# Kernel tuning notes

Measured on AMD Instinct MI355X. Metric: run time of the kernel, lower is better.

## Reference

```python
import jax, jax.numpy as jnp
import numpy as np

N = 50000       # nodes
E = 150000      # directed edges
NODE_IN = 64
EDGE_IN = 16
D = 32          # node_out_feats
EDGE_HID = 128
STEPS = 3       # num_step_message_passing


def setup_inputs() -> dict:
    key = jax.random.key(0)
    ks = jax.random.split(key, 10)
    s = 0.05
    return {
        "x": jax.random.normal(ks[0], (N, NODE_IN), jnp.float32),
        "edge_index": jax.random.randint(ks[1], (2, E), 0, N),
        "edge_attr": jax.random.normal(ks[2], (E, EDGE_IN), jnp.float32),
        # node_init Linear
        "Wn": jax.random.normal(ks[3], (NODE_IN, D), jnp.float32) * s,
        "bn": jnp.zeros((D,), jnp.float32),
        # edge_network: Linear(edge_in, hid) -> ReLU -> Linear(hid, D*D)
        "We1": jax.random.normal(ks[4], (EDGE_IN, EDGE_HID), jnp.float32) * s,
        "be1": jnp.zeros((EDGE_HID,), jnp.float32),
        "We2": jax.random.normal(ks[5], (EDGE_HID, D * D), jnp.float32) * s,
        "be2": jnp.zeros((D * D,), jnp.float32),
        # NNConv root weight + bias
        "Wroot": jax.random.normal(ks[6], (D, D), jnp.float32) * s,
        "bconv": jnp.zeros((D,), jnp.float32),
        # GRU (gate order r, z, n as in torch)
        "Wih": jax.random.normal(ks[7], (3 * D, D), jnp.float32) * s,
        "Whh": jax.random.normal(ks[8], (3 * D, D), jnp.float32) * s,
        "bih": jnp.zeros((3 * D,), jnp.float32),
        "bhh": jnp.zeros((3 * D,), jnp.float32),
    }


def _gru_cell(xt, h, Wih, Whh, bih, bhh):
    gi = xt @ Wih.T + bih   # [N, 3D]
    gh = h @ Whh.T + bhh    # [N, 3D]
    r = jax.nn.sigmoid(gi[:, :D] + gh[:, :D])
    z = jax.nn.sigmoid(gi[:, D:2 * D] + gh[:, D:2 * D])
    n = jnp.tanh(gi[:, 2 * D:] + r * gh[:, 2 * D:])
    return (1.0 - z) * n + z * h


def reference(x, edge_index, edge_attr, Wn, bn, We1, be1, We2, be2,
              Wroot, bconv, Wih, Whh, bih, bhh):
    src, dst = edge_index[0], edge_index[1]
    # per-edge weight matrices from edge_network (edge_attr fixed across steps)
    Wm = (jax.nn.relu(edge_attr @ We1 + be1) @ We2 + be2).reshape(E, D, D)
    h = jax.nn.relu(x @ Wn + bn)   # node_init
    hid = h                        # GRU hidden state
    for _ in range(STEPS):
        # NNConv: gather -> per-edge matmul -> scatter-add, plus root + bias
        m = jnp.einsum('ei,eio->eo', h[src], Wm)                # [E, D]
        agg = jax.ops.segment_sum(m, dst, num_segments=N)       # [N, D]
        conv = jax.nn.relu(agg + h @ Wroot + bconv)
        hid = _gru_cell(conv, hid, Wih, Whh, bih, bhh)
        h = hid
    return h
```

## Files before the change

### kernel.cpp

```cpp
#include <hip/hip_runtime.h>
#include <hip/hip_bf16.h>

#define N_NODES 50000
#define N_EDGES 150000
#define NODE_IN 64
#define EDGE_IN 16
#define DD 32
#define EHID 128
#define STEPS 3
#define EPB 64

__device__ __forceinline__ ushort f2b(float f) {
    __hip_bfloat16 b = __float2bfloat16(f);
    return *reinterpret_cast<ushort*>(&b);
}

typedef __bf16 bf16x8 __attribute__((ext_vector_type(8)));
typedef float  f32x4  __attribute__((ext_vector_type(4)));

#define LDA  136
#define HPAD 36

__global__ __launch_bounds__(256) void setup(const float* __restrict__ we2,
                                             const float* __restrict__ we1,
                                             const float* __restrict__ wroot,
                                             const float* __restrict__ wih,
                                             const float* __restrict__ whh,
                                             ushort* __restrict__ we2B,
                                             ushort* __restrict__ we1B,
                                             ushort* __restrict__ wgB,
                                             const float* __restrict__ x,
                                             const float* __restrict__ Wn,
                                             const float* __restrict__ bn,
                                             float* __restrict__ h) {
    __shared__ float Wns[NODE_IN * DD];
    __shared__ float bns[DD];
    int b = blockIdx.x, t = threadIdx.x;

    if (b < 70) {
        int i = b * 256 + t;
        if (i < 16384) {
            int l = i & 63, f = i >> 6;
            int kt = f & 3, nt = (f >> 2) & 3, bq = f >> 4;
            int lr = l & 15, lg = l >> 4;
            int n = bq * 64 + nt * 16 + lr;
            int k0 = kt * 32 + lg * 8;
            ushort tmp[8];
#pragma unroll
            for (int j = 0; j < 8; ++j) tmp[j] = f2b(we2[(size_t)(k0 + j) * 1024 + n]);
            *(uint4*)(we2B + (size_t)i * 8) = *(uint4*)tmp;
        } else if (i < 16896) {
            int u = i - 16384;
            int l = u & 63, nt = u >> 6;
            int lr = l & 15, lg = l >> 4;
            int n = nt * 16 + lr;
            ushort tmp[8];
#pragma unroll
            for (int j = 0; j < 8; ++j) {
                int k = lg * 8 + j;
                tmp[j] = (k < EDGE_IN) ? f2b(we1[(size_t)k * EHID + n]) : (ushort)0;
            }
            *(uint4*)(we1B + (size_t)u * 8) = *(uint4*)tmp;
        } else if (i < 17792) {
            int u = i - 16896;
            int l = u & 63;
            int lr = l & 15, lg = l >> 4;
            ushort tmp[8];
            if (u < 128) {
                int nt = u >> 6;
#pragma unroll
                for (int j = 0; j < 8; ++j)
                    tmp[j] = f2b(wroot[(size_t)(lg * 8 + j) * DD + nt * 16 + lr]);
            } else if (u < 512) {
                int nt = (u - 128) >> 6;
#pragma unroll
                for (int j = 0; j < 8; ++j)
                    tmp[j] = f2b(wih[(size_t)(nt * 16 + lr) * DD + lg * 8 + j]);
            } else {
                int nt = (u - 512) >> 6;
#pragma unroll
                for (int j = 0; j < 8; ++j)
                    tmp[j] = f2b(whh[(size_t)(nt * 16 + lr) * DD + lg * 8 + j]);
            }
            *(uint4*)(wgB + (size_t)u * 8) = *(uint4*)tmp;
        }
    } else {
        for (int i = t; i < NODE_IN * DD; i += 256) Wns[i] = Wn[i];
        if (t < DD) bns[t] = bn[t];
        __syncthreads();
        int n = (b - 70) * 256 + t;
        if (n >= N_NODES) return;
        float xr[NODE_IN];
        const float4* xp = (const float4*)(x + (size_t)n * NODE_IN);
#pragma unroll
        for (int q = 0; q < NODE_IN / 4; ++q) *(float4*)&xr[q * 4] = xp[q];
        float out[DD];
#pragma unroll
        for (int o = 0; o < DD; ++o) {
            float s = bns[o];
#pragma unroll
            for (int i = 0; i < NODE_IN; ++i) s += xr[i] * Wns[i * DD + o];
            out[o] = fmaxf(s, 0.f);
        }
        float4* hp = (float4*)(h + (size_t)n * DD);
#pragma unroll
        for (int q = 0; q < DD / 4; ++q) hp[q] = *(float4*)&out[q * 4];
    }
}

__global__ __launch_bounds__(256, 5) void fused_msg(const float* __restrict__ ea,
                                                    const ushort* __restrict__ we1B,
                                                    const float* __restrict__ be1,
                                                    const ushort* __restrict__ we2B,
                                                    const float* __restrict__ be2,
                                                    const int* __restrict__ ei,
                                                    const float* __restrict__ h,
                                                    float* __restrict__ agg) {
    __shared__ __attribute__((aligned(16))) ushort AsHs[12800];
    __shared__ float b1s[EHID];
    __shared__ float be2s[DD * DD];
    float* Hs = (float*)AsHs;
    ushort* Bs = AsHs + 4608;

    int t = threadIdx.x;
    if (t < EHID) b1s[t] = be1[t];
    for (int i = t; i < DD * DD; i += 256) be2s[i] = be2[i];

    int w = t >> 6, l = t & 63;
    int lr = l & 15, lg = l >> 4;
    int e0 = blockIdx.x * EPB;

    bf16x8 afe;
    {
        int e = e0 + w * 16 + lr;
        ushort tmp[8] = {0, 0, 0, 0, 0, 0, 0, 0};
        if (lg < 2 && e < N_EDGES) {
            const float4* p = (const float4*)(ea + (size_t)e * EDGE_IN + lg * 8);
            float4 a = p[0], b = p[1];
            tmp[0] = f2b(a.x); tmp[1] = f2b(a.y); tmp[2] = f2b(a.z); tmp[3] = f2b(a.w);
            tmp[4] = f2b(b.x); tmp[5] = f2b(b.y); tmp[6] = f2b(b.z); tmp[7] = f2b(b.w);
        }
        afe = *(bf16x8*)tmp;
    }
    __syncthreads();

#pragma unroll
    for (int nt = 0; nt < 8; ++nt) {
        bf16x8 bfe = *(const bf16x8*)(we1B + (size_t)((nt << 6) + l) * 8);
        int kh = nt * 16 + lr;
        float bb = b1s[kh];
        f32x4 acc = (f32x4){0.f, 0.f, 0.f, 0.f};
        acc = __builtin_amdgcn_mfma_f32_16x16x32_bf16(afe, bfe, acc, 0, 0, 0);
#pragma unroll
        for (int r = 0; r < 4; ++r)
            AsHs[(w * 16 + lg * 4 + r) * LDA + kh] = f2b(fmaxf(acc[r] + bb, 0.f));
    }
    __syncthreads();

    bf16x8 afrag[4];
#pragma unroll
    for (int kt = 0; kt < 4; ++kt)
        afrag[kt] = *(const bf16x8*)(&AsHs[(w * 16 + lr) * LDA + kt * 32 + lg * 8]);
    __syncthreads();

    {
        int row = t >> 2, qtr = t & 3;
        int e = e0 + row;
        float4* hd = (float4*)(Hs + row * HPAD) + qtr * 2;
        if (e < N_EDGES) {
            const float4* hr = (const float4*)(h + (size_t)ei[e] * DD) + qtr * 2;
            hd[0] = hr[0];
            hd[1] = hr[1];
        } else {
            float4 z = make_float4(0.f, 0.f, 0.f, 0.f);
            hd[0] = z; hd[1] = z;
        }
    }
#pragma unroll
    for (int q = 0; q < 4; ++q) {
        const ushort* gsrc = we2B + (size_t)(q * 256 + t) * 8;
        ushort* ldst = Bs + (size_t)(q * 256 + w * 64) * 8;
        __builtin_amdgcn_global_load_lds(
            (const __attribute__((address_space(1))) unsigned int*)gsrc,
            (__attribute__((address_space(3))) unsigned int*)ldst, 16, 0, 0);
    }
    asm volatile("s_waitcnt vmcnt(0)" ::: "memory");
    __syncthreads();

    float m_acc[4][2];
#pragma unroll
    for (int r = 0; r < 4; ++r) { m_acc[r][0] = 0.f; m_acc[r][1] = 0.f; }

    for (int bn = 0; bn < 16; ++bn) {
        float bv[4];
#pragma unroll
        for (int nt = 0; nt < 4; ++nt) bv[nt] = be2s[bn * 64 + nt * 16 + lr];

        f32x4 acc[4];
#pragma unroll
        for (int nt = 0; nt < 4; ++nt) acc[nt] = (f32x4){0.f, 0.f, 0.f, 0.f};

#pragma unroll
        for (int kt = 0; kt < 4; ++kt) {
            const ushort* base = Bs + (size_t)(kt * 64 + l) * 8;
            bf16x8 b0 = *(const bf16x8*)(base);
            bf16x8 b1 = *(const bf16x8*)(base + 2048);
            bf16x8 b2 = *(const bf16x8*)(base + 4096);
            bf16x8 b3 = *(const bf16x8*)(base + 6144);
            acc[0] = __builtin_amdgcn_mfma_f32_16x16x32_bf16(afrag[kt], b0, acc[0], 0, 0, 0);
            acc[1] = __builtin_amdgcn_mfma_f32_16x16x32_bf16(afrag[kt], b1, acc[1], 0, 0, 0);
            acc[2] = __builtin_amdgcn_mfma_f32_16x16x32_bf16(afrag[kt], b2, acc[2], 0, 0, 0);
            acc[3] = __builtin_amdgcn_mfma_f32_16x16x32_bf16(afrag[kt], b3, acc[3], 0, 0, 0);
        }

#pragma unroll
        for (int r = 0; r < 4; ++r) {
            int row = w * 16 + lg * 4 + r;
            float2 hv = *(const float2*)(Hs + row * HPAD + bn * 2);
#pragma unroll
            for (int nt = 0; nt < 4; ++nt) {
                float hi = (nt >> 1) ? hv.y : hv.x;
                m_acc[r][nt & 1] += hi * (acc[nt][r] + bv[nt]);
            }
        }

        if (bn < 15) {
            __syncthreads();
#pragma unroll
            for (int q = 0; q < 4; ++q) {
                const ushort* gsrc = we2B + (size_t)(bn + 1) * 8192 + (size_t)(q * 256 + t) * 8;
                ushort* ldst = Bs + (size_t)(q * 256 + w * 64) * 8;
                __builtin_amdgcn_global_load_lds(
                    (const __attribute__((address_space(1))) unsigned int*)gsrc,
                    (__attribute__((address_space(3))) unsigned int*)ldst, 16, 0, 0);
            }
            asm volatile("s_waitcnt vmcnt(0)" ::: "memory");
            __syncthreads();
        }
    }

#pragma unroll
    for (int r = 0; r < 4; ++r) {
        int le = w * 16 + lg * 4 + r;
        int e = e0 + le;
        if (e < N_EDGES) {
            int dst = ei[N_EDGES + e];
            float* ar = agg + (size_t)dst * DD;
            atomicAdd(ar + lr,      m_acc[r][0]);
            atomicAdd(ar + lr + 16, m_acc[r][1]);
        }
    }
}

__global__ __launch_bounds__(256) void conv_gru(float* agg,
                                                float* __restrict__ h,
                                                const ushort* __restrict__ wgB,
                                                const float* __restrict__ bconv,
                                                const float* __restrict__ bih,
                                                const float* __restrict__ bhh,
                                                float* out) {
    __shared__ __attribute__((aligned(16))) ushort Ah[64 * 40];
    __shared__ __attribute__((aligned(16))) ushort Ac[64 * 40];
    __shared__ float hs[64 * 33];
    __shared__ float bcs[DD], bis[3 * DD], bhs[3 * DD];
    int t = threadIdx.x;
    int base = blockIdx.x * 64;

    for (int idx = t; idx < 64 * DD; idx += 256) {
        int row = idx >> 5, col = idx & 31;
        int n = base + row;
        float v = (n < N_NODES) ? h[(size_t)n * DD + col] : 0.f;
        hs[row * 33 + col] = v;
        Ah[row * 40 + col] = f2b(v);
    }
    if (t < DD) bcs[t] = bconv[t];
    if (t < 3 * DD) { bis[t] = bih[t]; bhs[t] = bhh[t]; }
    __syncthreads();

    int w = t >> 6, l = t & 63;
    int lr = l & 15, lg = l >> 4;
    const f32x4 zro = (f32x4){0.f, 0.f, 0.f, 0.f};

    bf16x8 ah = *(const bf16x8*)(&Ah[(w * 16 + lr) * 40 + lg * 8]);

    f32x4 dcv[2];
#pragma unroll
    for (int nt = 0; nt < 2; ++nt) {
        bf16x8 b = *(const bf16x8*)(wgB + (size_t)(nt * 64 + l) * 8);
        dcv[nt] = __builtin_amdgcn_mfma_f32_16x16x32_bf16(ah, b, zro, 0, 0, 0);
    }
#pragma unroll
    for (int nt = 0; nt < 2; ++nt) {
#pragma unroll
        for (int r = 0; r < 4; ++r) {
            int row = w * 16 + lg * 4 + r;
            int col = nt * 16 + lr;
            int n = base + row;
            float a = 0.f;
            if (n < N_NODES) {
                a = agg[(size_t)n * DD + col];
                agg[(size_t)n * DD + col] = 0.f;
            }
            Ac[row * 40 + col] = f2b(fmaxf(dcv[nt][r] + a + bcs[col], 0.f));
        }
    }
    __syncthreads();

    bf16x8 ac = *(const bf16x8*)(&Ac[(w * 16 + lr) * 40 + lg * 8]);

    f32x4 gi[6], gh[6];
#pragma unroll
    for (int nt = 0; nt < 6; ++nt) {
        bf16x8 bi_ = *(const bf16x8*)(wgB + (size_t)(128 + nt * 64 + l) * 8);
        gi[nt] = __builtin_amdgcn_mfma_f32_16x16x32_bf16(ac, bi_, zro, 0, 0, 0);
        bf16x8 bh_ = *(const bf16x8*)(wgB + (size_t)(512 + nt * 64 + l) * 8);
        gh[nt] = __builtin_amdgcn_mfma_f32_16x16x32_bf16(ah, bh_, zro, 0, 0, 0);
    }

#pragma unroll
    for (int r = 0; r < 4; ++r) {
        int row = w * 16 + lg * 4 + r;
        int n = base + row;
        if (n >= N_NODES) continue;
#pragma unroll
        for (int ch = 0; ch < 2; ++ch) {
            int o = ch * 16 + lr;
            float girv = gi[ch][r]     + bis[o];
            float gizv = gi[2 + ch][r] + bis[DD + o];
            float ginv = gi[4 + ch][r] + bis[2 * DD + o];
            float ghrv = gh[ch][r]     + bhs[o];
            float ghzv = gh[2 + ch][r] + bhs[DD + o];
            float ghnv = gh[4 + ch][r] + bhs[2 * DD + o];
            float R  = 1.f / (1.f + expf(-(girv + ghrv)));
            float Z  = 1.f / (1.f + expf(-(gizv + ghzv)));
            float Nn = tanhf(ginv + R * ghnv);
            float hold = hs[row * 33 + o];
            float hnew = (1.f - Z) * Nn + Z * hold;
            h[(size_t)n * DD + o] = hnew;
            if (out) out[(size_t)n * DD + o] = hnew;
        }
    }
}

extern "C" void kernel_launch(void* const* d_in, const int* in_sizes, int n_in,
                              void* d_out, int out_size, void* d_ws, size_t ws_size,
                              hipStream_t stream) {
    const float* x    = (const float*)d_in[0];
    const int*   ei   = (const int*)d_in[1];
    const float* ea   = (const float*)d_in[2];
    const float* Wn   = (const float*)d_in[3];
    const float* bn   = (const float*)d_in[4];
    const float* We1  = (const float*)d_in[5];
    const float* be1  = (const float*)d_in[6];
    const float* We2  = (const float*)d_in[7];
    const float* be2  = (const float*)d_in[8];
    const float* Wroot= (const float*)d_in[9];
    const float* bconv= (const float*)d_in[10];
    const float* Wih  = (const float*)d_in[11];
    const float* Whh  = (const float*)d_in[12];
    const float* bih  = (const float*)d_in[13];
    const float* bhh  = (const float*)d_in[14];
    float* out = (float*)d_out;

    char* ws = (char*)d_ws;
    float*  h    = (float*)(ws);
    ushort* we2B = (ushort*)(ws + 6400000);
    ushort* we1B = (ushort*)(ws + 6662144);
    ushort* wgB  = (ushort*)(ws + 6670336);
    float*  agg  = (float*)d_out;

    setup<<<266, 256, 0, stream>>>(We2, We1, Wroot, Wih, Whh, we2B, we1B, wgB,
                                   x, Wn, bn, h);
    hipMemsetAsync(agg, 0, (size_t)N_NODES * DD * sizeof(float), stream);

    for (int step = 0; step < STEPS; ++step) {
        fused_msg<<<(N_EDGES + EPB - 1) / EPB, 256, 0, stream>>>(ea, we1B, be1, we2B, be2,
                                                                 ei, h, agg);
        conv_gru<<<(N_NODES + 63) / 64, 256, 0, stream>>>(agg, h, wgB, bconv, bih, bhh,
                                                          (step == STEPS - 1) ? out : nullptr);
    }
}
```

Measured before the change: 318.2 us.

## Fuse message passing steps into one persistent cooperative kernel with grid syncs

Replaces the six separate fused_msg and conv_gru launches with a single cooperative persistent kernel. It loops over the steps and uses grid-wide syncs between the edge message phase and the node GRU phase. This removes per-launch overhead and the idle tails between kernels. In exchange, the grid is capped by occupancy, so each block handles several edge tiles serially, and grid.sync plus threadfence add cost. The previous launch path stays as a fallback if the cooperative launch fails.

After: 1.162 ms. 265% more time.

```diff
diff --git a/kernel.cpp b/kernel.cpp
--- a/kernel.cpp
+++ b/kernel.cpp
@@ -1,5 +1,8 @@
 #include <hip/hip_runtime.h>
 #include <hip/hip_bf16.h>
+#include <hip/hip_cooperative_groups.h>
+
+namespace cg = cooperative_groups;
 
 #define N_NODES 50000
 #define N_EDGES 150000
@@ -9,6 +12,8 @@
 #define EHID 128
 #define STEPS 3
 #define EPB 64
+#define NFB ((N_EDGES + EPB - 1) / EPB)
+#define NCB ((N_NODES + 63) / 64)
 
 __device__ __forceinline__ ushort f2b(float f) {
     __hip_bfloat16 b = __float2bfloat16(f);
@@ -105,6 +110,254 @@
         float4* hp = (float4*)(h + (size_t)n * DD);
 #pragma unroll
         for (int q = 0; q < DD / 4; ++q) hp[q] = *(float4*)&out[q * 4];
+    }
+}
+
+__global__ __launch_bounds__(256, 5) void mpnn(const float* __restrict__ ea,
+                                               const ushort* __restrict__ we1B,
+                                               const float* __restrict__ be1,
+                                               const ushort* __restrict__ we2B,
+                                               const float* __restrict__ be2,
+                                               const int* __restrict__ ei,
+                                               float* __restrict__ h,
+                                               float* agg,
+                                               const ushort* __restrict__ wgB,
+                                               const float* __restrict__ bconv,
+                                               const float* __restrict__ bih,
+                                               const float* __restrict__ bhh,
+                                               float* out) {
+    cg::grid_group grid = cg::this_grid();
+
+    __shared__ __attribute__((aligned(16))) ushort SU[12800];
+    __shared__ float xb[1152];
+
+    int t = threadIdx.x;
+    int w = t >> 6, l = t & 63;
+    int lr = l & 15, lg = l >> 4;
+
+    float* b1s  = xb;
+    float* be2s = xb + 128;
+    float* bcs  = xb;
+    float* bis  = xb + 32;
+    float* bhs  = xb + 128;
+
+    for (int step = 0; step < STEPS; ++step) {
+        if (t < EHID) b1s[t] = be1[t];
+        for (int i = t; i < DD * DD; i += 256) be2s[i] = be2[i];
+
+        for (int vb = blockIdx.x; vb < NFB; vb += (int)gridDim.x) {
+            float* Hs = (float*)SU;
+            ushort* Bs = SU + 4608;
+            int e0 = vb * EPB;
+
+            bf16x8 afe;
+            {
+                int e = e0 + w * 16 + lr;
+                ushort tmp[8] = {0, 0, 0, 0, 0, 0, 0, 0};
+                if (lg < 2 && e < N_EDGES) {
+                    const float4* p = (const float4*)(ea + (size_t)e * EDGE_IN + lg * 8);
+                    float4 a = p[0], b = p[1];
+                    tmp[0] = f2b(a.x); tmp[1] = f2b(a.y); tmp[2] = f2b(a.z); tmp[3] = f2b(a.w);
+                    tmp[4] = f2b(b.x); tmp[5] = f2b(b.y); tmp[6] = f2b(b.z); tmp[7] = f2b(b.w);
+                }
+                afe = *(bf16x8*)tmp;
+            }
+            __syncthreads();
+
+#pragma unroll
+            for (int nt = 0; nt < 8; ++nt) {
+                bf16x8 bfe = *(const bf16x8*)(we1B + (size_t)((nt << 6) + l) * 8);
+                int kh = nt * 16 + lr;
+                float bb = b1s[kh];
+                f32x4 acc = (f32x4){0.f, 0.f, 0.f, 0.f};
+                acc = __builtin_amdgcn_mfma_f32_16x16x32_bf16(afe, bfe, acc, 0, 0, 0);
+#pragma unroll
+                for (int r = 0; r < 4; ++r)
+                    SU[(w * 16 + lg * 4 + r) * LDA + kh] = f2b(fmaxf(acc[r] + bb, 0.f));
+            }
+            __syncthreads();
+
+            bf16x8 afrag[4];
+#pragma unroll
+            for (int kt = 0; kt < 4; ++kt)
+                afrag[kt] = *(const bf16x8*)(&SU[(w * 16 + lr) * LDA + kt * 32 + lg * 8]);
+            __syncthreads();
+
+            {
+                int row = t >> 2, qtr = t & 3;
+                int e = e0 + row;
+                float4* hd = (float4*)(Hs + row * HPAD) + qtr * 2;
+                if (e < N_EDGES) {
+                    const float4* hr = (const float4*)(h + (size_t)ei[e] * DD) + qtr * 2;
+                    hd[0] = hr[0];
+                    hd[1] = hr[1];
+                } else {
+                    float4 z = make_float4(0.f, 0.f, 0.f, 0.f);
+                    hd[0] = z; hd[1] = z;
+                }
+            }
+#pragma unroll
+            for (int q = 0; q < 4; ++q) {
+                const ushort* gsrc = we2B + (size_t)(q * 256 + t) * 8;
+                ushort* ldst = Bs + (size_t)(q * 256 + w * 64) * 8;
+                __builtin_amdgcn_global_load_lds(
+                    (const __attribute__((address_space(1))) unsigned int*)gsrc,
+                    (__attribute__((address_space(3))) unsigned int*)ldst, 16, 0, 0);
+            }
+            asm volatile("s_waitcnt vmcnt(0)" ::: "memory");
+            __syncthreads();
+
+            float m_acc[4][2];
+#pragma unroll
+            for (int r = 0; r < 4; ++r) { m_acc[r][0] = 0.f; m_acc[r][1] = 0.f; }
+
+            for (int bn = 0; bn < 16; ++bn) {
+                float bv[4];
+#pragma unroll
+                for (int nt = 0; nt < 4; ++nt) bv[nt] = be2s[bn * 64 + nt * 16 + lr];
+
+                f32x4 acc[4];
+#pragma unroll
+                for (int nt = 0; nt < 4; ++nt) acc[nt] = (f32x4){0.f, 0.f, 0.f, 0.f};
+
+#pragma unroll
+                for (int kt = 0; kt < 4; ++kt) {
+                    const ushort* base = Bs + (size_t)(kt * 64 + l) * 8;
+                    bf16x8 b0 = *(const bf16x8*)(base);
+                    bf16x8 b1 = *(const bf16x8*)(base + 2048);
+                    bf16x8 b2 = *(const bf16x8*)(base + 4096);
+                    bf16x8 b3 = *(const bf16x8*)(base + 6144);
+                    acc[0] = __builtin_amdgcn_mfma_f32_16x16x32_bf16(afrag[kt], b0, acc[0], 0, 0, 0);
+                    acc[1] = __builtin_amdgcn_mfma_f32_16x16x32_bf16(afrag[kt], b1, acc[1], 0, 0, 0);
+                    acc[2] = __builtin_amdgcn_mfma_f32_16x16x32_bf16(afrag[kt], b2, acc[2], 0, 0, 0);
+                    acc[3] = __builtin_amdgcn_mfma_f32_16x16x32_bf16(afrag[kt], b3, acc[3], 0, 0, 0);
+                }
+
+#pragma unroll
+                for (int r = 0; r < 4; ++r) {
+                    int row = w * 16 + lg * 4 + r;
+                    float2 hv = *(const float2*)(Hs + row * HPAD + bn * 2);
+#pragma unroll
+                    for (int nt = 0; nt < 4; ++nt) {
+                        float hi = (nt >> 1) ? hv.y : hv.x;
+                        m_acc[r][nt & 1] += hi * (acc[nt][r] + bv[nt]);
+                    }
+                }
+
+                if (bn < 15) {
+                    __syncthreads();
+#pragma unroll
+                    for (int q = 0; q < 4; ++q) {
+                        const ushort* gsrc = we2B + (size_t)(bn + 1) * 8192 + (size_t)(q * 256 + t) * 8;
+                        ushort* ldst = Bs + (size_t)(q * 256 + w * 64) * 8;
+                        __builtin_amdgcn_global_load_lds(
+                            (const __attribute__((address_space(1))) unsigned int*)gsrc,
+                            (__attribute__((address_space(3))) unsigned int*)ldst, 16, 0, 0);
+                    }
+                    asm volatile("s_waitcnt vmcnt(0)" ::: "memory");
+                    __syncthreads();
+                }
+            }
+
+#pragma unroll
+            for (int r = 0; r < 4; ++r) {
+                int le = w * 16 + lg * 4 + r;
+                int e = e0 + le;
+                if (e < N_EDGES) {
+                    int dst = ei[N_EDGES + e];
+                    float* ar = agg + (size_t)dst * DD;
+                    atomicAdd(ar + lr,      m_acc[r][0]);
+                    atomicAdd(ar + lr + 16, m_acc[r][1]);
+                }
+            }
+        }
+        __threadfence();
+        grid.sync();
+
+        float* outp = (step == STEPS - 1) ? out : nullptr;
+        for (int vb = blockIdx.x; vb < NCB; vb += (int)gridDim.x) {
+            ushort* Ah = SU;
+            ushort* Ac = SU + 2560;
+            float*  hs = (float*)(SU + 5120);
+            int base = vb * 64;
+
+            __syncthreads();
+            for (int idx = t; idx < 64 * DD; idx += 256) {
+                int row = idx >> 5, col = idx & 31;
+                int n = base + row;
+                float v = (n < N_NODES) ? h[(size_t)n * DD + col] : 0.f;
+                hs[row * 33 + col] = v;
+                Ah[row * 40 + col] = f2b(v);
+            }
+            if (t < DD) bcs[t] = bconv[t];
+            if (t < 3 * DD) { bis[t] = bih[t]; bhs[t] = bhh[t]; }
+            __syncthreads();
+
+            const f32x4 zro = (f32x4){0.f, 0.f, 0.f, 0.f};
+            bf16x8 ah = *(const bf16x8*)(&Ah[(w * 16 + lr) * 40 + lg * 8]);
+
+            f32x4 dcv[2];
+#pragma unroll
+            for (int nt = 0; nt < 2; ++nt) {
+                bf16x8 b = *(const bf16x8*)(wgB + (size_t)(nt * 64 + l) * 8);
+                dcv[nt] = __builtin_amdgcn_mfma_f32_16x16x32_bf16(ah, b, zro, 0, 0, 0);
+            }
+#pragma unroll
+            for (int nt = 0; nt < 2; ++nt) {
+#pragma unroll
+                for (int r = 0; r < 4; ++r) {
+                    int row = w * 16 + lg * 4 + r;
+                    int col = nt * 16 + lr;
+                    int n = base + row;
+                    float a = 0.f;
+                    if (n < N_NODES) {
+                        a = agg[(size_t)n * DD + col];
+                        agg[(size_t)n * DD + col] = 0.f;
+                    }
+                    Ac[row * 40 + col] = f2b(fmaxf(dcv[nt][r] + a + bcs[col], 0.f));
+                }
+            }
+            __syncthreads();
+
+            bf16x8 ac = *(const bf16x8*)(&Ac[(w * 16 + lr) * 40 + lg * 8]);
+
+            f32x4 gi[6], gh[6];
+#pragma unroll
+            for (int nt = 0; nt < 6; ++nt) {
+                bf16x8 bi_ = *(const bf16x8*)(wgB + (size_t)(128 + nt * 64 + l) * 8);
+                gi[nt] = __builtin_amdgcn_mfma_f32_16x16x32_bf16(ac, bi_, zro, 0, 0, 0);
+                bf16x8 bh_ = *(const bf16x8*)(wgB + (size_t)(512 + nt * 64 + l) * 8);
+                gh[nt] = __builtin_amdgcn_mfma_f32_16x16x32_bf16(ah, bh_, zro, 0, 0, 0);
+            }
+
+#pragma unroll
+            for (int r = 0; r < 4; ++r) {
+                int row = w * 16 + lg * 4 + r;
+                int n = base + row;
+                if (n >= N_NODES) continue;
+#pragma unroll
+                for (int ch = 0; ch < 2; ++ch) {
+                    int o = ch * 16 + lr;
+                    float girv = gi[ch][r]     + bis[o];
+                    float gizv = gi[2 + ch][r] + bis[DD + o];
+                    float ginv = gi[4 + ch][r] + bis[2 * DD + o];
+                    float ghrv = gh[ch][r]     + bhs[o];
+                    float ghzv = gh[2 + ch][r] + bhs[DD + o];
+                    float ghnv = gh[4 + ch][r] + bhs[2 * DD + o];
+                    float R  = 1.f / (1.f + __expf(-(girv + ghrv)));
+                    float Z  = 1.f / (1.f + __expf(-(gizv + ghzv)));
+                    float xa = ginv + R * ghnv;
+                    float e2 = __expf(2.f * xa);
+                    float Nn = 1.f - 2.f / (e2 + 1.f);
+                    float hold = hs[row * 33 + o];
+                    float hnew = (1.f - Z) * Nn + Z * hold;
+                    h[(size_t)n * DD + o] = hnew;
+                    if (outp) outp[(size_t)n * DD + o] = hnew;
+                }
+            }
+        }
+        __threadfence();
+        grid.sync();
     }
 }
 
@@ -373,10 +626,33 @@
                                    x, Wn, bn, h);
     hipMemsetAsync(agg, 0, (size_t)N_NODES * DD * sizeof(float), stream);
 
-    for (int step = 0; step < STEPS; ++step) {
-        fused_msg<<<(N_EDGES + EPB - 1) / EPB, 256, 0, stream>>>(ea, we1B, be1, we2B, be2,
-                                                                 ei, h, agg);
-        conv_gru<<<(N_NODES + 63) / 64, 256, 0, stream>>>(agg, h, wgB, bconv, bih, bhh,
-                                                          (step == STEPS - 1) ? out : nullptr);
+    static int coopGrid = 0;
+    if (coopGrid == 0) {
+        int nb = 0;
+        if (hipOccupancyMaxActiveBlocksPerMultiprocessor(&nb, (const void*)mpnn, 256, 0)
+                != hipSuccess || nb < 1)
+            nb = 4;
+        hipDeviceProp_t prop;
+        int dev = 0;
+        hipGetDevice(&dev);
+        int cus = 256;
+        if (hipGetDeviceProperties(&prop, dev) == hipSuccess)
+            cus = prop.multiProcessorCount;
+        long g = (long)nb * cus;
+        if (g > NFB) g = NFB;
+        coopGrid = (int)g;
+    }
+
+    void* args[] = {(void*)&ea, (void*)&we1B, (void*)&be1, (void*)&we2B, (void*)&be2,
+                    (void*)&ei, (void*)&h, (void*)&agg, (void*)&wgB, (void*)&bconv,
+                    (void*)&bih, (void*)&bhh, (void*)&out};
+    hipError_t err = hipLaunchCooperativeKernel((const void*)mpnn, dim3(coopGrid),
+                                                dim3(256), args, 0, stream);
+    if (err != hipSuccess) {
+        for (int step = 0; step < STEPS; ++step) {
+            fused_msg<<<NFB, 256, 0, stream>>>(ea, we1B, be1, we2B, be2, ei, h, agg);
+            conv_gru<<<NCB, 256, 0, stream>>>(agg, h, wgB, bconv, bih, bhh,
+                                              (step == STEPS - 1) ? out : nullptr);
+        }
     }
 }
```
